# Performance work log

Hardware: AMD Instinct MI355X
Metric: run time of the kernel (lower is better)

## Reference

```python
import jax, jax.numpy as jnp
import numpy as np

N = 100000      # nodes
E = 1600000     # edges
IN, H, OUT = 128, 128, 64
P_DROP = 0.5


def _glorot_linear(key, out_d, in_d):
    # PyG Linear default init (kaiming-uniform-ish); exact init is irrelevant for the baseline
    bound = 1.0 / np.sqrt(in_d)
    return jax.random.uniform(key, (out_d, in_d), jnp.float32, -bound, bound)


def setup_inputs() -> dict:
    key = jax.random.key(0)
    ks = jax.random.split(key, 8)
    x = jax.random.normal(ks[0], (N, IN), jnp.float32)
    edge_index = jax.random.randint(ks[1], (2, E), 0, N, dtype=jnp.int64)
    W1l = _glorot_linear(ks[2], H, IN)
    b1 = jnp.zeros((H,), jnp.float32)
    W1r = _glorot_linear(ks[3], H, IN)
    W2l = _glorot_linear(ks[4], OUT, H)
    b2 = jnp.zeros((OUT,), jnp.float32)
    W2r = _glorot_linear(ks[5], OUT, H)
    return dict(x=x, edge_index=edge_index, W1l=W1l, b1=b1, W1r=W1r,
                W2l=W2l, b2=b2, W2r=W2r)


def _sage_conv(x, src, dst, Wl, bl, Wr):
    # PyG SAGEConv (aggr='mean'): out = lin_l(mean_{j in N(i)} x_j) + lin_r(x_i)
    msg = x[src]                                             # [E, d] gather
    agg = jax.ops.segment_sum(msg, dst, num_segments=N)      # [N, d] scatter-add
    cnt = jax.ops.segment_sum(jnp.ones((src.shape[0], 1), x.dtype), dst,
                              num_segments=N)                # [N, 1] in-degree
    mean = agg / jnp.maximum(cnt, 1.0)                       # isolated nodes -> 0
    return mean @ Wl.T + bl + x @ Wr.T


def reference(x, edge_index, W1l, b1, W1r, W2l, b2, W2r):
    src, dst = edge_index[0], edge_index[1]
    h = _sage_conv(x, src, dst, W1l, b1, W1r)
    h = jax.nn.relu(h)
    # F.dropout(p=0.5) made deterministic with a fixed key
    keep = jax.random.bernoulli(jax.random.key(42), 1.0 - P_DROP, h.shape)
    h = jnp.where(keep, h / (1.0 - P_DROP), 0.0)
    return _sage_conv(h, src, dst, W2l, b2, W2r)
```

## Files before the change

kernel.cpp:

```cpp
#include <hip/hip_runtime.h>
#include <hip/hip_bf16.h>

#define N_NODES 100000
#define NE      1600000

#define BINSH 7
#define NBIN  782
#define BCAP  3072
#define SEPB  16384
#define NBLK  ((NE + SEPB - 1) / SEPB)

typedef __attribute__((ext_vector_type(8))) short bfrag;
typedef __attribute__((ext_vector_type(4))) float ffrag;

#define BFLO(u) __uint_as_float((u) << 16)
#define BFHI(u) __uint_as_float((u) & 0xffff0000u)

__device__ __forceinline__ unsigned tf_rotl(unsigned x, int d) {
    return (x << d) | (x >> (32 - d));
}

__device__ __forceinline__ unsigned tf_word(unsigned f) {
    const unsigned ks0 = 0u;
    const unsigned ks1 = 42u;
    const unsigned ks2 = 0x1BD11BDAu ^ 0u ^ 42u;
    unsigned x0 = 0u + ks0;
    unsigned x1 = f + ks1;
#define TF_RND(r) { x0 += x1; x1 = tf_rotl(x1, r); x1 ^= x0; }
    TF_RND(13) TF_RND(15) TF_RND(26) TF_RND(6)
    x0 += ks1; x1 += ks2 + 1u;
    TF_RND(17) TF_RND(29) TF_RND(16) TF_RND(24)
    x0 += ks2; x1 += ks0 + 2u;
    TF_RND(13) TF_RND(15) TF_RND(26) TF_RND(6)
    x0 += ks0; x1 += ks1 + 3u;
    TF_RND(17) TF_RND(29) TF_RND(16) TF_RND(24)
    x0 += ks1; x1 += ks2 + 4u;
    TF_RND(13) TF_RND(15) TF_RND(26) TF_RND(6)
    x0 += ks2; x1 += ks0 + 5u;
#undef TF_RND
    return x0 ^ x1;
}

__device__ __forceinline__ unsigned short bf_bits(float v) {
    __hip_bfloat16 b = __float2bfloat16(v);
    return *(unsigned short*)&b;
}

__global__ void k_detect(const int* __restrict__ ei, int* __restrict__ flag) {
    __shared__ int nz;
    if (threadIdx.x == 0) nz = 0;
    __syncthreads();
    for (int i = threadIdx.x; i < 1024; i += blockDim.x)
        if (ei[2 * i + 1] != 0) atomicAdd(&nz, 1);
    __syncthreads();
    if (threadIdx.x == 0) *flag = (nz == 0) ? 1 : 0;
}

__global__ void k_conv(const float4* __restrict__ in, ushort4* __restrict__ out,
                       int n4) {
    int i = blockIdx.x * blockDim.x + threadIdx.x;
    if (i < n4) {
        float4 v = in[i];
        ushort4 o;
        o.x = bf_bits(v.x);
        o.y = bf_bits(v.y);
        o.z = bf_bits(v.z);
        o.w = bf_bits(v.w);
        out[i] = o;
    }
}

__global__ void k_wconv(const float* __restrict__ a, const float* __restrict__ b,
                        const float* __restrict__ c, const float* __restrict__ d,
                        __hip_bfloat16* __restrict__ o) {
    int i = blockIdx.x * blockDim.x + threadIdx.x;
    if (i < 16384)      o[i] = __float2bfloat16(a[i]);
    else if (i < 32768) o[i] = __float2bfloat16(b[i - 16384]);
    else if (i < 40960) o[i] = __float2bfloat16(c[i - 32768]);
    else if (i < 49152) o[i] = __float2bfloat16(d[i - 40960]);
}

__global__ __launch_bounds__(1024) void k_binscatter(const int* __restrict__ ei,
        const int* __restrict__ flag, int* __restrict__ bincur,
        int2* __restrict__ pairs) {
    __shared__ int h[NBIN];
    __shared__ int lbase[NBIN];
    for (int i = threadIdx.x; i < NBIN; i += 1024) h[i] = 0;
    __syncthreads();
    const int is64 = *flag;
    const int e0 = blockIdx.x * SEPB + threadIdx.x;
    int d[16], s[16];
#pragma unroll
    for (int k = 0; k < 16; ++k) {
        int e = e0 + k * 1024;
        if (e < NE) {
            d[k] = is64 ? ei[2 * (NE + e)] : ei[NE + e];
            s[k] = is64 ? ei[2 * e]        : ei[e];
            atomicAdd(&h[d[k] >> BINSH], 1);
        } else {
            d[k] = -1; s[k] = 0;
        }
    }
    __syncthreads();
    for (int i = threadIdx.x; i < NBIN; i += 1024) {
        int c = h[i];
        lbase[i] = c ? atomicAdd(&bincur[i], c) : 0;
        h[i] = 0;
    }
    __syncthreads();
#pragma unroll
    for (int k = 0; k < 16; ++k) {
        if (d[k] >= 0) {
            int b = d[k] >> BINSH;
            int r = atomicAdd(&h[b], 1);
            pairs[(size_t)b * BCAP + lbase[b] + r] = make_int2(s[k], d[k]);
        }
    }
}

__global__ __launch_bounds__(1024) void k_binscan(const int* __restrict__ bincnt,
        int* __restrict__ binptr) {
    __shared__ int sm[1024];
    const int t = threadIdx.x;
    int v = (t < NBIN) ? bincnt[t] : 0;
    sm[t] = v;
    __syncthreads();
    for (int off = 1; off < 1024; off <<= 1) {
        int u = (t >= off) ? sm[t - off] : 0;
        __syncthreads();
        sm[t] += u;
        __syncthreads();
    }
    if (t < NBIN) binptr[t] = sm[t] - v;
}

__global__ __launch_bounds__(256) void k_bin2csr(const int2* __restrict__ pairs,
        const int* __restrict__ binptr, const int* __restrict__ bincnt,
        int* __restrict__ ptr, int* __restrict__ adj) {
    __shared__ int cnt[128];
    __shared__ int sc[128];
    __shared__ int woff[128];
    const int b = blockIdx.x;
    const int base = binptr[b];
    const int nb = bincnt[b];
    const int2* pb = pairs + (size_t)b * BCAP;
    const int t = threadIdx.x;
    if (t < 128) cnt[t] = 0;
    __syncthreads();
    for (int i = t; i < nb; i += 256)
        atomicAdd(&cnt[pb[i].y & 127], 1);
    __syncthreads();
    if (t < 128) sc[t] = cnt[t];
    __syncthreads();
    for (int o = 1; o < 128; o <<= 1) {
        int u = 0;
        if (t < 128 && t >= o) u = sc[t - o];
        __syncthreads();
        if (t < 128) sc[t] += u;
        __syncthreads();
    }
    if (t < 128) {
        int ex = sc[t] - cnt[t];
        int node = b * 128 + t;
        if (node <= N_NODES) ptr[node] = base + ex;
        woff[t] = ex;
    }
    __syncthreads();
    for (int i = t; i < nb; i += 256) {
        int2 p = pb[i];
        int r = atomicAdd(&woff[p.y & 127], 1);
        adj[base + r] = p.x;
    }
}

__global__ void k_agg(const __hip_bfloat16* __restrict__ feat,
                      const int* __restrict__ ptr, const int* __restrict__ adj,
                      __hip_bfloat16* __restrict__ mean) {
    const int wid = (blockIdx.x * blockDim.x + threadIdx.x) >> 6;
    const int lane = threadIdx.x & 63;
    if (wid >= N_NODES) return;
    const int p0 = ptr[wid], p1 = ptr[wid + 1];
    float a0 = 0.f, b0 = 0.f, a1 = 0.f, b1 = 0.f;
    float a2 = 0.f, b2 = 0.f, a3 = 0.f, b3 = 0.f;
    int p = p0;
    for (; p + 7 < p1; p += 8) {
        int s0 = adj[p],     s1 = adj[p + 1], s2 = adj[p + 2], s3 = adj[p + 3];
        int s4 = adj[p + 4], s5 = adj[p + 5], s6 = adj[p + 6], s7 = adj[p + 7];
        unsigned u0 = *(const unsigned*)(feat + (size_t)s0 * 128 + lane * 2);
        unsigned u1 = *(const unsigned*)(feat + (size_t)s1 * 128 + lane * 2);
        unsigned u2 = *(const unsigned*)(feat + (size_t)s2 * 128 + lane * 2);
        unsigned u3 = *(const unsigned*)(feat + (size_t)s3 * 128 + lane * 2);
        unsigned u4 = *(const unsigned*)(feat + (size_t)s4 * 128 + lane * 2);
        unsigned u5 = *(const unsigned*)(feat + (size_t)s5 * 128 + lane * 2);
        unsigned u6 = *(const unsigned*)(feat + (size_t)s6 * 128 + lane * 2);
        unsigned u7 = *(const unsigned*)(feat + (size_t)s7 * 128 + lane * 2);
        a0 += BFLO(u0); b0 += BFHI(u0); a1 += BFLO(u1); b1 += BFHI(u1);
        a2 += BFLO(u2); b2 += BFHI(u2); a3 += BFLO(u3); b3 += BFHI(u3);
        a0 += BFLO(u4); b0 += BFHI(u4); a1 += BFLO(u5); b1 += BFHI(u5);
        a2 += BFLO(u6); b2 += BFHI(u6); a3 += BFLO(u7); b3 += BFHI(u7);
    }
    for (; p + 3 < p1; p += 4) {
        int s0 = adj[p], s1 = adj[p + 1], s2 = adj[p + 2], s3 = adj[p + 3];
        unsigned u0 = *(const unsigned*)(feat + (size_t)s0 * 128 + lane * 2);
        unsigned u1 = *(const unsigned*)(feat + (size_t)s1 * 128 + lane * 2);
        unsigned u2 = *(const unsigned*)(feat + (size_t)s2 * 128 + lane * 2);
        unsigned u3 = *(const unsigned*)(feat + (size_t)s3 * 128 + lane * 2);
        a0 += BFLO(u0); b0 += BFHI(u0); a1 += BFLO(u1); b1 += BFHI(u1);
        a2 += BFLO(u2); b2 += BFHI(u2); a3 += BFLO(u3); b3 += BFHI(u3);
    }
    for (; p < p1; ++p) {
        int s0 = adj[p];
        unsigned u0 = *(const unsigned*)(feat + (size_t)s0 * 128 + lane * 2);
        a0 += BFLO(u0); b0 += BFHI(u0);
    }
    const float inv = 1.0f / (float)max(p1 - p0, 1);
    float m0 = ((a0 + a1) + (a2 + a3)) * inv;
    float m1 = ((b0 + b1) + (b2 + b3)) * inv;
    unsigned o = ((unsigned)bf_bits(m1) << 16) | (unsigned)bf_bits(m0);
    *(unsigned*)(mean + (size_t)wid * 128 + lane * 2) = o;
}

__global__ void k_agg2(const __hip_bfloat16* __restrict__ feat,
                       const int* __restrict__ ptr, const int* __restrict__ adj,
                       __hip_bfloat16* __restrict__ mean) {
    const int node = (blockIdx.x * blockDim.x + threadIdx.x) >> 5;
    const int sl = threadIdx.x & 31;
    if (node >= N_NODES) return;
    const int p0 = ptr[node], p1 = ptr[node + 1];
    float a0 = 0.f, b0 = 0.f, a1 = 0.f, b1 = 0.f;
    float a2 = 0.f, b2 = 0.f, a3 = 0.f, b3 = 0.f;
    int p = p0;
    for (; p + 7 < p1; p += 8) {
        int s0 = adj[p],     s1 = adj[p + 1], s2 = adj[p + 2], s3 = adj[p + 3];
        int s4 = adj[p + 4], s5 = adj[p + 5], s6 = adj[p + 6], s7 = adj[p + 7];
        unsigned u0 = *(const unsigned*)(feat + (size_t)s0 * 64 + sl * 2);
        unsigned u1 = *(const unsigned*)(feat + (size_t)s1 * 64 + sl * 2);
        unsigned u2 = *(const unsigned*)(feat + (size_t)s2 * 64 + sl * 2);
        unsigned u3 = *(const unsigned*)(feat + (size_t)s3 * 64 + sl * 2);
        unsigned u4 = *(const unsigned*)(feat + (size_t)s4 * 64 + sl * 2);
        unsigned u5 = *(const unsigned*)(feat + (size_t)s5 * 64 + sl * 2);
        unsigned u6 = *(const unsigned*)(feat + (size_t)s6 * 64 + sl * 2);
        unsigned u7 = *(const unsigned*)(feat + (size_t)s7 * 64 + sl * 2);
        a0 += BFLO(u0); b0 += BFHI(u0); a1 += BFLO(u1); b1 += BFHI(u1);
        a2 += BFLO(u2); b2 += BFHI(u2); a3 += BFLO(u3); b3 += BFHI(u3);
        a0 += BFLO(u4); b0 += BFHI(u4); a1 += BFLO(u5); b1 += BFHI(u5);
        a2 += BFLO(u6); b2 += BFHI(u6); a3 += BFLO(u7); b3 += BFHI(u7);
    }
    for (; p + 3 < p1; p += 4) {
        int s0 = adj[p], s1 = adj[p + 1], s2 = adj[p + 2], s3 = adj[p + 3];
        unsigned u0 = *(const unsigned*)(feat + (size_t)s0 * 64 + sl * 2);
        unsigned u1 = *(const unsigned*)(feat + (size_t)s1 * 64 + sl * 2);
        unsigned u2 = *(const unsigned*)(feat + (size_t)s2 * 64 + sl * 2);
        unsigned u3 = *(const unsigned*)(feat + (size_t)s3 * 64 + sl * 2);
        a0 += BFLO(u0); b0 += BFHI(u0); a1 += BFLO(u1); b1 += BFHI(u1);
        a2 += BFLO(u2); b2 += BFHI(u2); a3 += BFLO(u3); b3 += BFHI(u3);
    }
    for (; p < p1; ++p) {
        int s0 = adj[p];
        unsigned u0 = *(const unsigned*)(feat + (size_t)s0 * 64 + sl * 2);
        a0 += BFLO(u0); b0 += BFHI(u0);
    }
    const float inv = 1.0f / (float)max(p1 - p0, 1);
    float m0 = ((a0 + a1) + (a2 + a3)) * inv;
    float m1 = ((b0 + b1) + (b2 + b3)) * inv;
    unsigned o = ((unsigned)bf_bits(m1) << 16) | (unsigned)bf_bits(m0);
    *(unsigned*)(mean + (size_t)node * 64 + sl * 2) = o;
}

__global__ __launch_bounds__(256) void k_lin1(
    const __hip_bfloat16* __restrict__ Am, const __hip_bfloat16* __restrict__ Ax,
    const __hip_bfloat16* __restrict__ Wl, const __hip_bfloat16* __restrict__ Wr,
    const float* __restrict__ bias, __hip_bfloat16* __restrict__ out) {
    const int tid = threadIdx.x;
    const int w  = tid >> 6;
    const int l  = tid & 63;
    const int lr = l & 15;
    const int lk = l >> 4;
    const int j0 = w * 32;
    const int n0 = blockIdx.x * 64;

    bfrag B[2][2][4];
#pragma unroll
    for (int jt = 0; jt < 2; ++jt) {
        const int jrow = j0 + jt * 16 + lr;
#pragma unroll
        for (int ks = 0; ks < 4; ++ks) {
            B[jt][0][ks] = *(const bfrag*)(Wl + jrow * 128 + ks * 32 + lk * 8);
            B[jt][1][ks] = *(const bfrag*)(Wr + jrow * 128 + ks * 32 + lk * 8);
        }
    }
    const float bj0 = bias[j0 + lr];
    const float bj1 = bias[j0 + 16 + lr];

    for (int t = 0; t < 4; ++t) {
        const int rbase = n0 + t * 16;
        int arow = rbase + lr;
        if (arow > N_NODES - 1) arow = N_NODES - 1;
        ffrag acc0 = {0.f, 0.f, 0.f, 0.f};
        ffrag acc1 = {0.f, 0.f, 0.f, 0.f};
#pragma unroll
        for (int ks = 0; ks < 4; ++ks) {
            bfrag am = *(const bfrag*)(Am + (size_t)arow * 128 + ks * 32 + lk * 8);
            bfrag ax = *(const bfrag*)(Ax + (size_t)arow * 128 + ks * 32 + lk * 8);
            acc0 = __builtin_amdgcn_mfma_f32_16x16x32_bf16(am, B[0][0][ks], acc0, 0, 0, 0);
            acc1 = __builtin_amdgcn_mfma_f32_16x16x32_bf16(am, B[1][0][ks], acc1, 0, 0, 0);
            acc0 = __builtin_amdgcn_mfma_f32_16x16x32_bf16(ax, B[0][1][ks], acc0, 0, 0, 0);
            acc1 = __builtin_amdgcn_mfma_f32_16x16x32_bf16(ax, B[1][1][ks], acc1, 0, 0, 0);
        }
#pragma unroll
        for (int r = 0; r < 4; ++r) {
            const int n = rbase + lk * 4 + r;
            if (n < N_NODES) {
                float v0 = fmaxf(acc0[r] + bj0, 0.f);
                unsigned rb0 = tf_word((unsigned)(n * 128 + j0 + lr));
                v0 = (rb0 & 0x80000000u) ? 0.f : (v0 + v0);
                out[(size_t)n * 128 + j0 + lr] = __float2bfloat16(v0);
                float v1 = fmaxf(acc1[r] + bj1, 0.f);
                unsigned rb1 = tf_word((unsigned)(n * 128 + j0 + 16 + lr));
                v1 = (rb1 & 0x80000000u) ? 0.f : (v1 + v1);
                out[(size_t)n * 128 + j0 + 16 + lr] = __float2bfloat16(v1);
            }
        }
    }
}

__global__ __launch_bounds__(256) void k_y2(
    const __hip_bfloat16* __restrict__ Ah, const __hip_bfloat16* __restrict__ Wl,
    __hip_bfloat16* __restrict__ y2) {
    const int tid = threadIdx.x;
    const int w  = tid >> 6;
    const int l  = tid & 63;
    const int lr = l & 15;
    const int lk = l >> 4;
    const int j0 = w * 16;
    const int n0 = blockIdx.x * 64;

    bfrag Bl[4];
    const int jrow = j0 + lr;
#pragma unroll
    for (int ks = 0; ks < 4; ++ks)
        Bl[ks] = *(const bfrag*)(Wl + jrow * 128 + ks * 32 + lk * 8);

    for (int t = 0; t < 4; ++t) {
        const int rbase = n0 + t * 16;
        int arow = rbase + lr;
        if (arow > N_NODES - 1) arow = N_NODES - 1;
        ffrag acc = {0.f, 0.f, 0.f, 0.f};
#pragma unroll
        for (int ks = 0; ks < 4; ++ks) {
            bfrag ah = *(const bfrag*)(Ah + (size_t)arow * 128 + ks * 32 + lk * 8);
            acc = __builtin_amdgcn_mfma_f32_16x16x32_bf16(ah, Bl[ks], acc, 0, 0, 0);
        }
#pragma unroll
        for (int r = 0; r < 4; ++r) {
            const int n = rbase + lk * 4 + r;
            if (n < N_NODES)
                y2[(size_t)n * 64 + j0 + lr] = __float2bfloat16(acc[r]);
        }
    }
}

__global__ __launch_bounds__(256) void k_lin2(
    const __hip_bfloat16* __restrict__ M2, const __hip_bfloat16* __restrict__ Ah,
    const __hip_bfloat16* __restrict__ Wr, const float* __restrict__ bias,
    float* __restrict__ out) {
    const int tid = threadIdx.x;
    const int w  = tid >> 6;
    const int l  = tid & 63;
    const int lr = l & 15;
    const int lk = l >> 4;
    const int j0 = w * 16;
    const int n0 = blockIdx.x * 64;

    bfrag Br[4];
    const int jrow = j0 + lr;
#pragma unroll
    for (int ks = 0; ks < 4; ++ks)
        Br[ks] = *(const bfrag*)(Wr + jrow * 128 + ks * 32 + lk * 8);
    const float bj = bias[j0 + lr];

    for (int t = 0; t < 4; ++t) {
        const int rbase = n0 + t * 16;
        int arow = rbase + lr;
        if (arow > N_NODES - 1) arow = N_NODES - 1;
        ffrag acc = {0.f, 0.f, 0.f, 0.f};
#pragma unroll
        for (int ks = 0; ks < 4; ++ks) {
            bfrag ah = *(const bfrag*)(Ah + (size_t)arow * 128 + ks * 32 + lk * 8);
            acc = __builtin_amdgcn_mfma_f32_16x16x32_bf16(ah, Br[ks], acc, 0, 0, 0);
        }
#pragma unroll
        for (int r = 0; r < 4; ++r) {
            const int n = rbase + lk * 4 + r;
            if (n < N_NODES) {
                float m = __bfloat162float(M2[(size_t)n * 64 + j0 + lr]);
                out[(size_t)n * 64 + j0 + lr] = acc[r] + bj + m;
            }
        }
    }
}

extern "C" void kernel_launch(void* const* d_in, const int* in_sizes, int n_in,
                              void* d_out, int out_size, void* d_ws, size_t ws_size,
                              hipStream_t stream) {
    const float* x   = (const float*)d_in[0];
    const int*   ei  = (const int*)d_in[1];
    const float* W1l = (const float*)d_in[2];
    const float* b1  = (const float*)d_in[3];
    const float* W1r = (const float*)d_in[4];
    const float* W2l = (const float*)d_in[5];
    const float* b2  = (const float*)d_in[6];
    const float* W2r = (const float*)d_in[7];
    float* out = (float*)d_out;

    char* w = (char*)d_ws;
    int* flag   = (int*)w;
    int* bincur = flag + 64;
    int* binptr = bincur + 1024;
    int* ptr    = binptr + 1024;
    int* adj    = ptr + (N_NODES + 1);
    size_t foff = (((size_t)(64 + 1024 + 1024 + N_NODES + 1 + NE)) * 4 + 255)
                  & ~(size_t)255;
    __hip_bfloat16* wb    = (__hip_bfloat16*)(w + foff);
    __hip_bfloat16* w1lb  = wb;
    __hip_bfloat16* w1rb  = wb + 16384;
    __hip_bfloat16* w2lb  = wb + 32768;
    __hip_bfloat16* w2rb  = wb + 40960;
    __hip_bfloat16* xb    = wb + 49152;
    __hip_bfloat16* meanb = xb + (size_t)N_NODES * 128;
    __hip_bfloat16* hb    = meanb + (size_t)N_NODES * 128;
    int2* pairs = (int2*)hb;
    __hip_bfloat16* y2b = meanb;
    __hip_bfloat16* m2b = meanb + (size_t)N_NODES * 64;

    hipMemsetAsync(bincur, 0, 1024 * sizeof(int), stream);

    const int n4 = N_NODES * 128 / 4;
    k_conv<<<(n4 + 255) / 256, 256, 0, stream>>>((const float4*)x, (ushort4*)xb, n4);
    k_wconv<<<192, 256, 0, stream>>>(W1l, W1r, W2l, W2r, wb);

    k_detect<<<1, 256, 0, stream>>>(ei, flag);

    k_binscatter<<<NBLK, 1024, 0, stream>>>(ei, flag, bincur, pairs);
    k_binscan<<<1, 1024, 0, stream>>>(bincur, binptr);
    k_bin2csr<<<NBIN, 256, 0, stream>>>(pairs, binptr, bincur, ptr, adj);

    const int ab = (N_NODES + 3) / 4;
    const int nb = (N_NODES + 63) / 64;
    const int ab2 = (N_NODES + 7) / 8;

    k_agg<<<ab, 256, 0, stream>>>(xb, ptr, adj, meanb);
    k_lin1<<<nb, 256, 0, stream>>>(meanb, xb, w1lb, w1rb, b1, hb);
    k_y2<<<nb, 256, 0, stream>>>(hb, w2lb, y2b);
    k_agg2<<<ab2, 256, 0, stream>>>(y2b, ptr, adj, m2b);
    k_lin2<<<nb, 256, 0, stream>>>(m2b, hb, w2rb, b2, out);
}
```

Measured before the change: 254.0 us.

## Fuse layer-1 linear with layer-2 projections and precompute dropout bitmask

Merges the layer-1 linear (with ReLU and dropout), the layer-2 left projection and the layer-2 root linear into one kernel. The dropout-activated hidden tile stays in LDS instead of being written to and reread from global memory. The final aggregation kernel now adds the neighbour mean directly into the output, which already holds the root term. Dropout bits come from a separate kernel that computes each Threefry word once and packs the keep flags into 64-bit ballot masks, so the GEMM epilogue no longer runs the hash per element. In exchange, the output is read and written twice, and an extra mask kernel runs before the graph build.

Result: no change. 249.3 us (-1.9%).

```diff
diff --git a/kernel.cpp b/kernel.cpp
--- a/kernel.cpp
+++ b/kernel.cpp
@@ -9,6 +9,7 @@
 #define BCAP  3072
 #define SEPB  16384
 #define NBLK  ((NE + SEPB - 1) / SEPB)
+#define NMASKW 200000
 
 typedef __attribute__((ext_vector_type(8))) short bfrag;
 typedef __attribute__((ext_vector_type(4))) float ffrag;
@@ -44,6 +45,17 @@
 __device__ __forceinline__ unsigned short bf_bits(float v) {
     __hip_bfloat16 b = __float2bfloat16(v);
     return *(unsigned short*)&b;
+}
+
+__global__ void k_mask(unsigned long long* __restrict__ km) {
+    const int lane = threadIdx.x & 63;
+    const int w0 = (blockIdx.x * blockDim.x + threadIdx.x) >> 6;
+    const int nw = (gridDim.x * blockDim.x) >> 6;
+    for (int widx = w0; widx < NMASKW; widx += nw) {
+        unsigned wv = tf_word((unsigned)widx * 64u + (unsigned)lane);
+        unsigned long long keep = __ballot(!(wv & 0x80000000u));
+        if (lane == 0) km[widx] = keep;
+    }
 }
 
 __global__ void k_detect(const int* __restrict__ ei, int* __restrict__ flag) {
@@ -220,9 +232,98 @@
     *(unsigned*)(mean + (size_t)wid * 128 + lane * 2) = o;
 }
 
-__global__ void k_agg2(const __hip_bfloat16* __restrict__ feat,
-                       const int* __restrict__ ptr, const int* __restrict__ adj,
-                       __hip_bfloat16* __restrict__ mean) {
+__global__ __launch_bounds__(256) void k_lin1f(
+    const __hip_bfloat16* __restrict__ Am, const __hip_bfloat16* __restrict__ Ax,
+    const __hip_bfloat16* __restrict__ W1l, const __hip_bfloat16* __restrict__ W1r,
+    const float* __restrict__ b1,
+    const __hip_bfloat16* __restrict__ W2l, const __hip_bfloat16* __restrict__ W2r,
+    const float* __restrict__ b2,
+    const unsigned long long* __restrict__ kmask,
+    __hip_bfloat16* __restrict__ y2, float* __restrict__ zout) {
+    __shared__ __align__(16) __hip_bfloat16 hs[64][136];
+    const int tid = threadIdx.x;
+    const int w  = tid >> 6;
+    const int l  = tid & 63;
+    const int lr = l & 15;
+    const int lk = l >> 4;
+    const int j0 = w * 32;
+    const int j2 = w * 16 + lr;
+    const int n0 = blockIdx.x * 64;
+
+    bfrag B1[2][2][4];
+#pragma unroll
+    for (int jt = 0; jt < 2; ++jt) {
+        const int jrow = j0 + jt * 16 + lr;
+#pragma unroll
+        for (int ks = 0; ks < 4; ++ks) {
+            B1[jt][0][ks] = *(const bfrag*)(W1l + jrow * 128 + ks * 32 + lk * 8);
+            B1[jt][1][ks] = *(const bfrag*)(W1r + jrow * 128 + ks * 32 + lk * 8);
+        }
+    }
+    bfrag Bl2[4], Br2[4];
+#pragma unroll
+    for (int ks = 0; ks < 4; ++ks) {
+        Bl2[ks] = *(const bfrag*)(W2l + j2 * 128 + ks * 32 + lk * 8);
+        Br2[ks] = *(const bfrag*)(W2r + j2 * 128 + ks * 32 + lk * 8);
+    }
+    const float bj0 = b1[j0 + lr];
+    const float bj1 = b1[j0 + 16 + lr];
+    const float bj2 = b2[j2];
+
+    for (int t = 0; t < 4; ++t) {
+        const int rbase = n0 + t * 16;
+        int arow = rbase + lr;
+        if (arow > N_NODES - 1) arow = N_NODES - 1;
+        ffrag acc0 = {0.f, 0.f, 0.f, 0.f};
+        ffrag acc1 = {0.f, 0.f, 0.f, 0.f};
+#pragma unroll
+        for (int ks = 0; ks < 4; ++ks) {
+            bfrag am = *(const bfrag*)(Am + (size_t)arow * 128 + ks * 32 + lk * 8);
+            bfrag ax = *(const bfrag*)(Ax + (size_t)arow * 128 + ks * 32 + lk * 8);
+            acc0 = __builtin_amdgcn_mfma_f32_16x16x32_bf16(am, B1[0][0][ks], acc0, 0, 0, 0);
+            acc1 = __builtin_amdgcn_mfma_f32_16x16x32_bf16(am, B1[1][0][ks], acc1, 0, 0, 0);
+            acc0 = __builtin_amdgcn_mfma_f32_16x16x32_bf16(ax, B1[0][1][ks], acc0, 0, 0, 0);
+            acc1 = __builtin_amdgcn_mfma_f32_16x16x32_bf16(ax, B1[1][1][ks], acc1, 0, 0, 0);
+        }
+#pragma unroll
+        for (int r = 0; r < 4; ++r) {
+            const int n = rbase + lk * 4 + r;
+            const int lrow = t * 16 + lk * 4 + r;
+            const int nm = (n < N_NODES) ? n : (N_NODES - 1);
+            const unsigned long long km = kmask[nm * 2 + (j0 >> 6)];
+            float v0 = fmaxf(acc0[r] + bj0, 0.f);
+            v0 = ((km >> ((j0 + lr) & 63)) & 1ull) ? (v0 + v0) : 0.f;
+            hs[lrow][j0 + lr] = __float2bfloat16(v0);
+            float v1 = fmaxf(acc1[r] + bj1, 0.f);
+            v1 = ((km >> ((j0 + 16 + lr) & 63)) & 1ull) ? (v1 + v1) : 0.f;
+            hs[lrow][j0 + 16 + lr] = __float2bfloat16(v1);
+        }
+    }
+    __syncthreads();
+
+    for (int t = 0; t < 4; ++t) {
+        ffrag accY = {0.f, 0.f, 0.f, 0.f};
+        ffrag accZ = {0.f, 0.f, 0.f, 0.f};
+#pragma unroll
+        for (int ks = 0; ks < 4; ++ks) {
+            bfrag ah = *(const bfrag*)&hs[t * 16 + lr][ks * 32 + lk * 8];
+            accY = __builtin_amdgcn_mfma_f32_16x16x32_bf16(ah, Bl2[ks], accY, 0, 0, 0);
+            accZ = __builtin_amdgcn_mfma_f32_16x16x32_bf16(ah, Br2[ks], accZ, 0, 0, 0);
+        }
+#pragma unroll
+        for (int r = 0; r < 4; ++r) {
+            const int n = n0 + t * 16 + lk * 4 + r;
+            if (n < N_NODES) {
+                y2[(size_t)n * 64 + j2]   = __float2bfloat16(accY[r]);
+                zout[(size_t)n * 64 + j2] = accZ[r] + bj2;
+            }
+        }
+    }
+}
+
+__global__ void k_agg2f(const __hip_bfloat16* __restrict__ feat,
+                        const int* __restrict__ ptr, const int* __restrict__ adj,
+                        float* __restrict__ out) {
     const int node = (blockIdx.x * blockDim.x + threadIdx.x) >> 5;
     const int sl = threadIdx.x & 31;
     if (node >= N_NODES) return;
@@ -263,141 +364,11 @@
     const float inv = 1.0f / (float)max(p1 - p0, 1);
     float m0 = ((a0 + a1) + (a2 + a3)) * inv;
     float m1 = ((b0 + b1) + (b2 + b3)) * inv;
-    unsigned o = ((unsigned)bf_bits(m1) << 16) | (unsigned)bf_bits(m0);
-    *(unsigned*)(mean + (size_t)node * 64 + sl * 2) = o;
-}
-
-__global__ __launch_bounds__(256) void k_lin1(
-    const __hip_bfloat16* __restrict__ Am, const __hip_bfloat16* __restrict__ Ax,
-    const __hip_bfloat16* __restrict__ Wl, const __hip_bfloat16* __restrict__ Wr,
-    const float* __restrict__ bias, __hip_bfloat16* __restrict__ out) {
-    const int tid = threadIdx.x;
-    const int w  = tid >> 6;
-    const int l  = tid & 63;
-    const int lr = l & 15;
-    const int lk = l >> 4;
-    const int j0 = w * 32;
-    const int n0 = blockIdx.x * 64;
-
-    bfrag B[2][2][4];
-#pragma unroll
-    for (int jt = 0; jt < 2; ++jt) {
-        const int jrow = j0 + jt * 16 + lr;
-#pragma unroll
-        for (int ks = 0; ks < 4; ++ks) {
-            B[jt][0][ks] = *(const bfrag*)(Wl + jrow * 128 + ks * 32 + lk * 8);
-            B[jt][1][ks] = *(const bfrag*)(Wr + jrow * 128 + ks * 32 + lk * 8);
-        }
-    }
-    const float bj0 = bias[j0 + lr];
-    const float bj1 = bias[j0 + 16 + lr];
-
-    for (int t = 0; t < 4; ++t) {
-        const int rbase = n0 + t * 16;
-        int arow = rbase + lr;
-        if (arow > N_NODES - 1) arow = N_NODES - 1;
-        ffrag acc0 = {0.f, 0.f, 0.f, 0.f};
-        ffrag acc1 = {0.f, 0.f, 0.f, 0.f};
-#pragma unroll
-        for (int ks = 0; ks < 4; ++ks) {
-            bfrag am = *(const bfrag*)(Am + (size_t)arow * 128 + ks * 32 + lk * 8);
-            bfrag ax = *(const bfrag*)(Ax + (size_t)arow * 128 + ks * 32 + lk * 8);
-            acc0 = __builtin_amdgcn_mfma_f32_16x16x32_bf16(am, B[0][0][ks], acc0, 0, 0, 0);
-            acc1 = __builtin_amdgcn_mfma_f32_16x16x32_bf16(am, B[1][0][ks], acc1, 0, 0, 0);
-            acc0 = __builtin_amdgcn_mfma_f32_16x16x32_bf16(ax, B[0][1][ks], acc0, 0, 0, 0);
-            acc1 = __builtin_amdgcn_mfma_f32_16x16x32_bf16(ax, B[1][1][ks], acc1, 0, 0, 0);
-        }
-#pragma unroll
-        for (int r = 0; r < 4; ++r) {
-            const int n = rbase + lk * 4 + r;
-            if (n < N_NODES) {
-                float v0 = fmaxf(acc0[r] + bj0, 0.f);
-                unsigned rb0 = tf_word((unsigned)(n * 128 + j0 + lr));
-                v0 = (rb0 & 0x80000000u) ? 0.f : (v0 + v0);
-                out[(size_t)n * 128 + j0 + lr] = __float2bfloat16(v0);
-                float v1 = fmaxf(acc1[r] + bj1, 0.f);
-                unsigned rb1 = tf_word((unsigned)(n * 128 + j0 + 16 + lr));
-                v1 = (rb1 & 0x80000000u) ? 0.f : (v1 + v1);
-                out[(size_t)n * 128 + j0 + 16 + lr] = __float2bfloat16(v1);
-            }
-        }
-    }
-}
-
-__global__ __launch_bounds__(256) void k_y2(
-    const __hip_bfloat16* __restrict__ Ah, const __hip_bfloat16* __restrict__ Wl,
-    __hip_bfloat16* __restrict__ y2) {
-    const int tid = threadIdx.x;
-    const int w  = tid >> 6;
-    const int l  = tid & 63;
-    const int lr = l & 15;
-    const int lk = l >> 4;
-    const int j0 = w * 16;
-    const int n0 = blockIdx.x * 64;
-
-    bfrag Bl[4];
-    const int jrow = j0 + lr;
-#pragma unroll
-    for (int ks = 0; ks < 4; ++ks)
-        Bl[ks] = *(const bfrag*)(Wl + jrow * 128 + ks * 32 + lk * 8);
-
-    for (int t = 0; t < 4; ++t) {
-        const int rbase = n0 + t * 16;
-        int arow = rbase + lr;
-        if (arow > N_NODES - 1) arow = N_NODES - 1;
-        ffrag acc = {0.f, 0.f, 0.f, 0.f};
-#pragma unroll
-        for (int ks = 0; ks < 4; ++ks) {
-            bfrag ah = *(const bfrag*)(Ah + (size_t)arow * 128 + ks * 32 + lk * 8);
-            acc = __builtin_amdgcn_mfma_f32_16x16x32_bf16(ah, Bl[ks], acc, 0, 0, 0);
-        }
-#pragma unroll
-        for (int r = 0; r < 4; ++r) {
-            const int n = rbase + lk * 4 + r;
-            if (n < N_NODES)
-                y2[(size_t)n * 64 + j0 + lr] = __float2bfloat16(acc[r]);
-        }
-    }
-}
-
-__global__ __launch_bounds__(256) void k_lin2(
-    const __hip_bfloat16* __restrict__ M2, const __hip_bfloat16* __restrict__ Ah,
-    const __hip_bfloat16* __restrict__ Wr, const float* __restrict__ bias,
-    float* __restrict__ out) {
-    const int tid = threadIdx.x;
-    const int w  = tid >> 6;
-    const int l  = tid & 63;
-    const int lr = l & 15;
-    const int lk = l >> 4;
-    const int j0 = w * 16;
-    const int n0 = blockIdx.x * 64;
-
-    bfrag Br[4];
-    const int jrow = j0 + lr;
-#pragma unroll
-    for (int ks = 0; ks < 4; ++ks)
-        Br[ks] = *(const bfrag*)(Wr + jrow * 128 + ks * 32 + lk * 8);
-    const float bj = bias[j0 + lr];
-
-    for (int t = 0; t < 4; ++t) {
-        const int rbase = n0 + t * 16;
-        int arow = rbase + lr;
-        if (arow > N_NODES - 1) arow = N_NODES - 1;
-        ffrag acc = {0.f, 0.f, 0.f, 0.f};
-#pragma unroll
-        for (int ks = 0; ks < 4; ++ks) {
-            bfrag ah = *(const bfrag*)(Ah + (size_t)arow * 128 + ks * 32 + lk * 8);
-            acc = __builtin_amdgcn_mfma_f32_16x16x32_bf16(ah, Br[ks], acc, 0, 0, 0);
-        }
-#pragma unroll
-        for (int r = 0; r < 4; ++r) {
-            const int n = rbase + lk * 4 + r;
-            if (n < N_NODES) {
-                float m = __bfloat162float(M2[(size_t)n * 64 + j0 + lr]);
-                out[(size_t)n * 64 + j0 + lr] = acc[r] + bj + m;
-            }
-        }
-    }
+    float2 z = *(const float2*)(out + (size_t)node * 64 + sl * 2);
+    float2 o;
+    o.x = z.x + m0;
+    o.y = z.y + m1;
+    *(float2*)(out + (size_t)node * 64 + sl * 2) = o;
 }
 
 extern "C" void kernel_launch(void* const* d_in, const int* in_sizes, int n_in,
@@ -419,8 +390,10 @@
     int* binptr = bincur + 1024;
     int* ptr    = binptr + 1024;
     int* adj    = ptr + (N_NODES + 1);
-    size_t foff = (((size_t)(64 + 1024 + 1024 + N_NODES + 1 + NE)) * 4 + 255)
+    size_t koff = (((size_t)(64 + 1024 + 1024 + N_NODES + 1 + NE)) * 4 + 255)
                   & ~(size_t)255;
+    unsigned long long* kmask = (unsigned long long*)(w + koff);
+    size_t foff = (koff + (size_t)NMASKW * 8 + 255) & ~(size_t)255;
     __hip_bfloat16* wb    = (__hip_bfloat16*)(w + foff);
     __hip_bfloat16* w1lb  = wb;
     __hip_bfloat16* w1rb  = wb + 16384;
@@ -428,30 +401,28 @@
     __hip_bfloat16* w2rb  = wb + 40960;
     __hip_bfloat16* xb    = wb + 49152;
     __hip_bfloat16* meanb = xb + (size_t)N_NODES * 128;
-    __hip_bfloat16* hb    = meanb + (size_t)N_NODES * 128;
-    int2* pairs = (int2*)hb;
-    __hip_bfloat16* y2b = meanb;
-    __hip_bfloat16* m2b = meanb + (size_t)N_NODES * 64;
+    char* pregion = (char*)(meanb + (size_t)N_NODES * 128);
+    int2* pairs = (int2*)pregion;
+    __hip_bfloat16* y2b = (__hip_bfloat16*)pregion;
 
     hipMemsetAsync(bincur, 0, 1024 * sizeof(int), stream);
 
     const int n4 = N_NODES * 128 / 4;
     k_conv<<<(n4 + 255) / 256, 256, 0, stream>>>((const float4*)x, (ushort4*)xb, n4);
     k_wconv<<<192, 256, 0, stream>>>(W1l, W1r, W2l, W2r, wb);
-
     k_detect<<<1, 256, 0, stream>>>(ei, flag);
+    k_mask<<<1024, 256, 0, stream>>>(kmask);
 
     k_binscatter<<<NBLK, 1024, 0, stream>>>(ei, flag, bincur, pairs);
     k_binscan<<<1, 1024, 0, stream>>>(bincur, binptr);
     k_bin2csr<<<NBIN, 256, 0, stream>>>(pairs, binptr, bincur, ptr, adj);
 
-    const int ab = (N_NODES + 3) / 4;
-    const int nb = (N_NODES + 63) / 64;
+    const int ab  = (N_NODES + 3) / 4;
+    const int nb  = (N_NODES + 63) / 64;
     const int ab2 = (N_NODES + 7) / 8;
 
     k_agg<<<ab, 256, 0, stream>>>(xb, ptr, adj, meanb);
-    k_lin1<<<nb, 256, 0, stream>>>(meanb, xb, w1lb, w1rb, b1, hb);
-    k_y2<<<nb, 256, 0, stream>>>(hb, w2lb, y2b);
-    k_agg2<<<ab2, 256, 0, stream>>>(y2b, ptr, adj, m2b);
-    k_lin2<<<nb, 256, 0, stream>>>(m2b, hb, w2rb, b2, out);
-}
+    k_lin1f<<<nb, 256, 0, stream>>>(meanb, xb, w1lb, w1rb, b1,
+                                    w2lb, w2rb, b2, kmask, y2b, out);
+    k_agg2f<<<ab2, 256, 0, stream>>>(y2b, ptr, adj, out);
+}
```
